# Performance work log

Measured on AMD Instinct MI355X. Metric: run time of the kernel, lower is better.

## Reference

```python
import jax, jax.numpy as jnp
import numpy as np

N, E, D, B, C = 50000, 800000, 128, 20000, 40
EPS_BN = 1e-3    # keras BatchNormalization default epsilon
EPS_NRM = 1e-12  # keras ops.nn.normalize epsilon
FFN_DIMS = {"pre": (D, D), "c1p": (D, D), "c1u": (2 * D, D), "c2p": (D, D), "c2u": (2 * D, D), "post": (D, D)}


def setup_inputs() -> dict:
    key = jax.random.key(0)
    ks = jax.random.split(key, 8)
    inp = {
        "node_features": jax.random.normal(ks[0], (N, D), jnp.float32),
        "edges": jax.random.randint(ks[1], (2, E), 0, N, dtype=jnp.int32),
        "edge_w": jax.random.uniform(ks[2], (E,), jnp.float32),
        "input_node_idx": jax.random.randint(ks[3], (B,), 0, N, dtype=jnp.int32),
    }
    for i, (name, (din, dout)) in enumerate(FFN_DIMS.items()):
        kw = jax.random.fold_in(key, 100 + i)
        inp[name + "_g"] = jnp.ones((din,), jnp.float32)
        inp[name + "_be"] = jnp.zeros((din,), jnp.float32)
        inp[name + "_mu"] = jnp.zeros((din,), jnp.float32)
        inp[name + "_var"] = jnp.ones((din,), jnp.float32)
        inp[name + "_w"] = jax.random.normal(kw, (din, dout), jnp.float32) * (1.0 / float(np.sqrt(din)))
        inp[name + "_bi"] = jnp.zeros((dout,), jnp.float32)
    inp["logits_w"] = jax.random.normal(ks[4], (D, C), jnp.float32) * (1.0 / float(np.sqrt(D)))
    inp["logits_b"] = jnp.zeros((C,), jnp.float32)
    return inp


def ffn(x, g, be, mu, var, w, bi):
    # BatchNorm (inference running stats) -> Dropout (identity) -> Dense + exact gelu
    xn = (x - mu) * jax.lax.rsqrt(var + EPS_BN) * g + be
    return jax.nn.gelu(xn @ w + bi, approximate=False)


def l2norm(x):
    n = jnp.sqrt(jnp.sum(x * x, axis=-1, keepdims=True))
    return x / jnp.maximum(n, EPS_NRM)


def graph_conv(x, node_idx, nbr_idx, ew, prep, upd):
    # gather neighbours -> prepare FFN -> edge-weighted -> segment_sum (reduce='sum')
    msgs = ffn(x[nbr_idx], *prep) * ew[:, None]                         # [E, D]
    red = jax.ops.segment_sum(msgs, node_idx, num_segments=x.shape[0])  # [N, D]
    h = jnp.concatenate([x, red], axis=1)                               # [N, 2D] (combination='concat')
    return l2norm(ffn(h, *upd))                                         # normalize=True


def reference(node_features, edges, edge_w, input_node_idx,
              pre_g, pre_be, pre_mu, pre_var, pre_w, pre_bi,
              c1p_g, c1p_be, c1p_mu, c1p_var, c1p_w, c1p_bi,
              c1u_g, c1u_be, c1u_mu, c1u_var, c1u_w, c1u_bi,
              c2p_g, c2p_be, c2p_mu, c2p_var, c2p_w, c2p_bi,
              c2u_g, c2u_be, c2u_mu, c2u_var, c2u_w, c2u_bi,
              post_g, post_be, post_mu, post_var, post_w, post_bi,
              logits_w, logits_b):
    ew = edge_w / jnp.sum(edge_w)                       # edge_W normalized at init
    node_idx, nbr_idx = edges[0], edges[1]
    x = ffn(node_features, pre_g, pre_be, pre_mu, pre_var, pre_w, pre_bi)
    x = graph_conv(x, node_idx, nbr_idx, ew,
                   (c1p_g, c1p_be, c1p_mu, c1p_var, c1p_w, c1p_bi),
                   (c1u_g, c1u_be, c1u_mu, c1u_var, c1u_w, c1u_bi)) + x
    x = graph_conv(x, node_idx, nbr_idx, ew,
                   (c2p_g, c2p_be, c2p_mu, c2p_var, c2p_w, c2p_bi),
                   (c2u_g, c2u_be, c2u_mu, c2u_var, c2u_w, c2u_bi)) + x
    x = ffn(x, post_g, post_be, post_mu, post_var, post_w, post_bi)
    return x[input_node_idx] @ logits_w + logits_b      # [B, C]
```

## Files before the change

kernel.cpp:

```cpp
#include <hip/hip_runtime.h>
#include <hip/hip_fp16.h>
#include <math.h>

static constexpr int D = 128;
static constexpr int CAP = 64;
static constexpr float EPS_BN = 1e-3f;

typedef short short8 __attribute__((ext_vector_type(8)));
typedef short short4v __attribute__((ext_vector_type(4)));
typedef float float4v __attribute__((ext_vector_type(4)));

__device__ __forceinline__ float gelu_exact(float x) {
    return 0.5f * x * (1.0f + erff(x * 0.70710678118654752f));
}

__device__ __forceinline__ void f32_to_hilo(float f, short& h, short& l) {
    unsigned u = __float_as_uint(f);
    h = (short)(u >> 16);
    float hf = __uint_as_float(u & 0xFFFF0000u);
    unsigned lu = __float_as_uint(f - hf);
    l = (short)(lu >> 16);
}

__device__ __forceinline__ short f32_to_bf16_rne(float f) {
    unsigned u = __float_as_uint(f);
    u += 0x7FFFu + ((u >> 16) & 1u);
    return (short)(u >> 16);
}

__global__ void k_fill_bucket(const int* __restrict__ edges, const float* __restrict__ ew,
                              int* __restrict__ cnt, float* __restrict__ sums,
                              unsigned* __restrict__ cw, int E) {
    int e = blockIdx.x * blockDim.x + threadIdx.x;
    float s = 0.f;
    if (e < E) {
        int dst = edges[e], src = edges[E + e];
        float w = ew[e];
        s = w;
        unsigned short wb = __half_as_ushort(__float2half(w));
        int idx = atomicAdd(&cnt[dst], 1);
        if (idx < CAP)
            cw[(size_t)dst * CAP + idx] = ((unsigned)src << 16) | (unsigned)wb;
    }
    for (int off = 32; off > 0; off >>= 1) s += __shfl_down(s, off, 64);
    __shared__ float sm[4];
    int lane = threadIdx.x & 63, wv = threadIdx.x >> 6;
    if (lane == 0) sm[wv] = s;
    __syncthreads();
    if (threadIdx.x == 0) atomicAdd(sums, sm[0] + sm[1] + sm[2] + sm[3]);
}

struct FoldArgs {
    const float* g[6]; const float* be[6]; const float* mu[6];
    const float* var[6]; const float* w[6]; const float* bi[6];
    short* wh[6]; short* wl[6]; float* bp[6]; int K[6];
};

__global__ void k_fold_all(FoldArgs fa) {
    const int f = blockIdx.y;
    const int c = blockIdx.x;
    const int K = fa.K[f];
    const float* g = fa.g[f]; const float* be = fa.be[f];
    const float* mu = fa.mu[f]; const float* var = fa.var[f];
    const float* w = fa.w[f]; const float* bi = fa.bi[f];
    short* wh = fa.wh[f]; short* wl = fa.wl[f]; float* bp = fa.bp[f];
    float part = 0.f;
    for (int k = threadIdx.x; k < K; k += blockDim.x) {
        float a = g[k] / sqrtf(var[k] + EPS_BN);
        float wv = w[k * D + c];
        float prod = a * wv;
        short hh, ll;
        f32_to_hilo(prod, hh, ll);
        wh[c * K + k] = hh;
        wl[c * K + k] = ll;
        part += (be[k] - mu[k] * a) * wv;
    }
    for (int off = 32; off > 0; off >>= 1) part += __shfl_down(part, off, 64);
    __shared__ float sm[4];
    int lane = threadIdx.x & 63, wv_ = threadIdx.x >> 6;
    if (lane == 0) sm[wv_] = part;
    __syncthreads();
    if (threadIdx.x == 0) bp[c] = bi[c] + sm[0] + sm[1] + sm[2] + sm[3];
}

__global__ void k_reduce(const int* __restrict__ cnt, const unsigned* __restrict__ cw,
                         const float* __restrict__ sums, const __half* __restrict__ y,
                         float* __restrict__ red, int N) {
    int n = blockIdx.x * (blockDim.x >> 6) + (threadIdx.x >> 6);
    if (n >= N) return;
    float inv = 1.0f / sums[0];
    int lane = threadIdx.x & 63;
    int sub = lane >> 4;
    int q = lane & 15;
    int count = min(cnt[n], CAP);
    int start = n * CAP;
    int end = start + count;
    float acc[8] = {0.f, 0.f, 0.f, 0.f, 0.f, 0.f, 0.f, 0.f};
    int i = start + sub;
    if (i < end) {
        unsigned c = cw[i];
        for (;;) {
            int ni = i + 4;
            unsigned nc = 0;
            if (ni < end) nc = cw[ni];
            int src = (int)(c >> 16);
            float w = __half2float(__ushort_as_half((unsigned short)(c & 0xFFFFu))) * inv;
            float4 raw = *((const float4*)(y + (size_t)src * D) + q);
            const __half2* hp = (const __half2*)&raw;
            #pragma unroll
            for (int t = 0; t < 4; t++) {
                float2 f = __half22float2(hp[t]);
                acc[t * 2]     += w * f.x;
                acc[t * 2 + 1] += w * f.y;
            }
            if (ni >= end) break;
            i = ni; c = nc;
        }
    }
    #pragma unroll
    for (int t = 0; t < 8; t++) {
        acc[t] += __shfl_xor(acc[t], 16, 64);
        acc[t] += __shfl_xor(acc[t], 32, 64);
    }
    if (sub == 0) {
        float4 o0 = {acc[0], acc[1], acc[2], acc[3]};
        float4 o1 = {acc[4], acc[5], acc[6], acc[7]};
        *((float4*)(red + (size_t)n * D + q * 8)) = o0;
        *((float4*)(red + (size_t)n * D + q * 8 + 4)) = o1;
    }
}

template<int K, bool L2RES, bool OUT16, bool SPLIT3>
__device__ __forceinline__ void ffn_body(
    short (*__restrict__ Abuf)[128][72], short (*__restrict__ Wbuf)[128][72],
    float (*__restrict__ rs)[2],
    const float* __restrict__ A0, const float* __restrict__ A1,
    const short* __restrict__ Wh, const short* __restrict__ Wl,
    const float* __restrict__ bp, const float* __restrict__ resid,
    float* __restrict__ outf, __half* __restrict__ outh, int nrows)
{
    const int tid = threadIdx.x;
    const int lane = tid & 63;
    const int wv = tid >> 6;
    const int wr = wv >> 1;
    const int wc = wv & 1;
    const int m = lane & 15;
    const int quad = lane >> 4;
    const int rowBlock = blockIdx.x * 128;

    float4v acc[4][4];
    #pragma unroll
    for (int ti = 0; ti < 4; ti++)
        #pragma unroll
        for (int tj = 0; tj < 4; tj++)
            acc[ti][tj] = (float4v){0.f, 0.f, 0.f, 0.f};

    for (int cc = 0; cc < K / 64; cc++) {
        const float* Asrc = (K == 256 && cc >= 2) ? A1 : A0;
        const int kb = (K == 256) ? ((cc & 1) * 64) : (cc * 64);
        const int kw = cc * 64;

        #pragma unroll
        for (int t = 0; t < 8; t++) {
            int i = tid + t * 256;
            int r = i >> 4, k4 = i & 15;
            int grow = rowBlock + r; if (grow >= nrows) grow = nrows - 1;
            float4 f = *((const float4*)(Asrc + (size_t)grow * D + kb) + k4);
            if (SPLIT3) {
                short h0, l0, h1, l1, h2, l2, h3, l3;
                f32_to_hilo(f.x, h0, l0);
                f32_to_hilo(f.y, h1, l1);
                f32_to_hilo(f.z, h2, l2);
                f32_to_hilo(f.w, h3, l3);
                short4v hh = {h0, h1, h2, h3};
                short4v ll = {l0, l1, l2, l3};
                *(short4v*)&Abuf[0][r][k4 * 4] = hh;
                *(short4v*)&Abuf[1][r][k4 * 4] = ll;
            } else {
                short4v hh = {f32_to_bf16_rne(f.x), f32_to_bf16_rne(f.y),
                              f32_to_bf16_rne(f.z), f32_to_bf16_rne(f.w)};
                *(short4v*)&Abuf[0][r][k4 * 4] = hh;
            }
        }
        #pragma unroll
        for (int t = 0; t < 4; t++) {
            int i = tid + t * 256;
            int c = i >> 3, g = i & 7;
            short8 wh8 = *(const short8*)(Wh + (size_t)c * K + kw + g * 8);
            *(short8*)&Wbuf[0][c][g * 8] = wh8;
            if (SPLIT3) {
                short8 wl8 = *(const short8*)(Wl + (size_t)c * K + kw + g * 8);
                *(short8*)&Wbuf[1][c][g * 8] = wl8;
            }
        }
        __syncthreads();

        #pragma unroll
        for (int ks = 0; ks < 2; ks++) {
            short8 ah[4], bh[4];
            #pragma unroll
            for (int ti = 0; ti < 4; ti++)
                ah[ti] = *(const short8*)&Abuf[0][wr * 64 + ti * 16 + m][ks * 32 + quad * 8];
            #pragma unroll
            for (int tj = 0; tj < 4; tj++)
                bh[tj] = *(const short8*)&Wbuf[0][wc * 64 + tj * 16 + m][ks * 32 + quad * 8];
            if (SPLIT3) {
                short8 al[4], bl[4];
                #pragma unroll
                for (int ti = 0; ti < 4; ti++)
                    al[ti] = *(const short8*)&Abuf[1][wr * 64 + ti * 16 + m][ks * 32 + quad * 8];
                #pragma unroll
                for (int tj = 0; tj < 4; tj++)
                    bl[tj] = *(const short8*)&Wbuf[1][wc * 64 + tj * 16 + m][ks * 32 + quad * 8];
                #pragma unroll
                for (int ti = 0; ti < 4; ti++)
                    #pragma unroll
                    for (int tj = 0; tj < 4; tj++) {
                        acc[ti][tj] = __builtin_amdgcn_mfma_f32_16x16x32_bf16(al[ti], bh[tj], acc[ti][tj], 0, 0, 0);
                        acc[ti][tj] = __builtin_amdgcn_mfma_f32_16x16x32_bf16(ah[ti], bl[tj], acc[ti][tj], 0, 0, 0);
                        acc[ti][tj] = __builtin_amdgcn_mfma_f32_16x16x32_bf16(ah[ti], bh[tj], acc[ti][tj], 0, 0, 0);
                    }
            } else {
                #pragma unroll
                for (int ti = 0; ti < 4; ti++)
                    #pragma unroll
                    for (int tj = 0; tj < 4; tj++)
                        acc[ti][tj] = __builtin_amdgcn_mfma_f32_16x16x32_bf16(ah[ti], bh[tj], acc[ti][tj], 0, 0, 0);
            }
        }
        __syncthreads();
    }

    float bvv[4];
    #pragma unroll
    for (int tj = 0; tj < 4; tj++) bvv[tj] = bp[wc * 64 + tj * 16 + m];

    float g[4][4][4];
    #pragma unroll
    for (int ti = 0; ti < 4; ti++)
        #pragma unroll
        for (int tj = 0; tj < 4; tj++)
            #pragma unroll
            for (int r4 = 0; r4 < 4; r4++)
                g[ti][tj][r4] = gelu_exact(acc[ti][tj][r4] + bvv[tj]);

    if (L2RES) {
        #pragma unroll
        for (int ti = 0; ti < 4; ti++)
            #pragma unroll
            for (int r4 = 0; r4 < 4; r4++) {
                float ss = 0.f;
                #pragma unroll
                for (int tj = 0; tj < 4; tj++) ss += g[ti][tj][r4] * g[ti][tj][r4];
                ss += __shfl_xor(ss, 1, 64);
                ss += __shfl_xor(ss, 2, 64);
                ss += __shfl_xor(ss, 4, 64);
                ss += __shfl_xor(ss, 8, 64);
                if (m == 0) rs[wr * 64 + ti * 16 + quad * 4 + r4][wc] = ss;
            }
        __syncthreads();
        #pragma unroll
        for (int ti = 0; ti < 4; ti++)
            #pragma unroll
            for (int r4 = 0; r4 < 4; r4++) {
                int rib = wr * 64 + ti * 16 + quad * 4 + r4;
                float tot = rs[rib][0] + rs[rib][1];
                float inv = 1.0f / fmaxf(sqrtf(tot), 1e-12f);
                int row = rowBlock + rib;
                if (row < nrows) {
                    #pragma unroll
                    for (int tj = 0; tj < 4; tj++) {
                        int c = wc * 64 + tj * 16 + m;
                        outf[(size_t)row * D + c] = g[ti][tj][r4] * inv + resid[(size_t)row * D + c];
                    }
                }
            }
    } else {
        #pragma unroll
        for (int ti = 0; ti < 4; ti++)
            #pragma unroll
            for (int r4 = 0; r4 < 4; r4++) {
                int row = rowBlock + wr * 64 + ti * 16 + quad * 4 + r4;
                if (row < nrows) {
                    #pragma unroll
                    for (int tj = 0; tj < 4; tj++) {
                        int c = wc * 64 + tj * 16 + m;
                        if (OUT16) outh[(size_t)row * D + c] = __float2half(g[ti][tj][r4]);
                        else       outf[(size_t)row * D + c] = g[ti][tj][r4];
                    }
                }
            }
    }
}

__global__ __launch_bounds__(256, 2) void k_pair1(
    const float* __restrict__ nf,
    const short* __restrict__ Wh0, const short* __restrict__ Wl0, const float* __restrict__ Bp0,
    float* __restrict__ xA,
    const short* __restrict__ Wh1, const float* __restrict__ Bp1,
    __half* __restrict__ yh, int N)
{
    __shared__ short Abuf[2][128][72];
    __shared__ short Wbuf[2][128][72];
    __shared__ float rs[128][2];
    ffn_body<128, false, false, true>(Abuf, Wbuf, rs, nf, nullptr, Wh0, Wl0, Bp0, nullptr, xA, nullptr, N);
    __syncthreads();
    ffn_body<128, false, true, false>(Abuf, Wbuf, rs, xA, nullptr, Wh1, nullptr, Bp1, nullptr, nullptr, yh, N);
}

__global__ __launch_bounds__(256, 2) void k_pair2(
    const float* __restrict__ xA, const float* __restrict__ red,
    const short* __restrict__ Wh2, const short* __restrict__ Wl2, const float* __restrict__ Bp2,
    float* __restrict__ y,
    const short* __restrict__ Wh3, const float* __restrict__ Bp3,
    __half* __restrict__ yh, int N)
{
    __shared__ short Abuf[2][128][72];
    __shared__ short Wbuf[2][128][72];
    __shared__ float rs[128][2];
    ffn_body<256, true, false, true>(Abuf, Wbuf, rs, xA, red, Wh2, Wl2, Bp2, xA, y, nullptr, N);
    __syncthreads();
    ffn_body<128, false, true, false>(Abuf, Wbuf, rs, y, nullptr, Wh3, nullptr, Bp3, nullptr, nullptr, yh, N);
}

__global__ __launch_bounds__(256, 2) void k_pair3(
    const float* __restrict__ y, const float* __restrict__ red_in,
    const short* __restrict__ Wh4, const short* __restrict__ Wl4, const float* __restrict__ Bp4,
    float* __restrict__ xA,
    const short* __restrict__ Wh5, const short* __restrict__ Wl5, const float* __restrict__ Bp5,
    float* __restrict__ yout, int N)
{
    __shared__ short Abuf[2][128][72];
    __shared__ short Wbuf[2][128][72];
    __shared__ float rs[128][2];
    ffn_body<256, true, false, true>(Abuf, Wbuf, rs, y, red_in, Wh4, Wl4, Bp4, y, xA, nullptr, N);
    __syncthreads();
    ffn_body<128, false, false, true>(Abuf, Wbuf, rs, xA, nullptr, Wh5, Wl5, Bp5, nullptr, yout, nullptr, N);
}

__global__ void k_logits(const float* __restrict__ x, const int* __restrict__ idx,
                         const float* __restrict__ LW, const float* __restrict__ lb,
                         float* __restrict__ out, int B) {
    int wid = blockIdx.x * 4 + (threadIdx.x >> 6);
    int lane = threadIdx.x & 63;
    if (wid >= B) return;
    int row = __builtin_amdgcn_readfirstlane(idx[wid]);
    if (lane >= 40) return;
    float acc = lb[lane];
    const float4* xr = (const float4*)(x + (size_t)row * D);
    #pragma unroll 4
    for (int k4 = 0; k4 < 32; k4++) {
        float4 xv = xr[k4];
        acc += xv.x * LW[(4 * k4 + 0) * 40 + lane];
        acc += xv.y * LW[(4 * k4 + 1) * 40 + lane];
        acc += xv.z * LW[(4 * k4 + 2) * 40 + lane];
        acc += xv.w * LW[(4 * k4 + 3) * 40 + lane];
    }
    out[(size_t)wid * 40 + lane] = acc;
}

extern "C" void kernel_launch(void* const* d_in, const int* in_sizes, int n_in,
                              void* d_out, int out_size, void* d_ws, size_t ws_size,
                              hipStream_t stream) {
    const float* node_features = (const float*)d_in[0];
    const int*   edges         = (const int*)d_in[1];
    const float* edge_w        = (const float*)d_in[2];
    const int*   input_idx     = (const int*)d_in[3];
    const int N = in_sizes[0] / D;
    const int E = in_sizes[2];
    const int B = in_sizes[3];

    const float* P[6][6];
    for (int f = 0; f < 6; f++)
        for (int q = 0; q < 6; q++)
            P[f][q] = (const float*)d_in[4 + f * 6 + q];
    const float* logits_w = (const float*)d_in[40];
    const float* logits_b = (const float*)d_in[41];

    float* ws = (float*)d_ws;
    size_t nd = (size_t)N * D;
    float* xA  = ws;
    float* y   = ws + nd;
    float* red = ws + 2 * nd;
    float* p   = ws + 3 * nd;
    __half* yh = (__half*)p; p += nd / 2;
    const int Ks[6] = {128, 128, 256, 128, 256, 128};
    short* Wh[6]; short* Wl[6]; float* Bp[6];
    {
        short* sp = (short*)p;
        for (int f = 0; f < 6; f++) {
            Wh[f] = sp; sp += (size_t)Ks[f] * D;
            Wl[f] = sp; sp += (size_t)Ks[f] * D;
        }
        p = (float*)sp;
    }
    for (int f = 0; f < 6; f++) { Bp[f] = p; p += D; }
    int* cnt    = (int*)p; p += N;
    float* sums = p; p += 2;
    unsigned* cw = (unsigned*)p; p += (size_t)N * CAP;

    hipMemsetAsync(cnt, 0, ((size_t)N + 2) * sizeof(int), stream);
    k_fill_bucket<<<(E + 255) / 256, 256, 0, stream>>>(edges, edge_w, cnt, sums, cw, E);

    FoldArgs fa;
    for (int f = 0; f < 6; f++) {
        fa.g[f] = P[f][0]; fa.be[f] = P[f][1]; fa.mu[f] = P[f][2];
        fa.var[f] = P[f][3]; fa.w[f] = P[f][4]; fa.bi[f] = P[f][5];
        fa.wh[f] = Wh[f]; fa.wl[f] = Wl[f]; fa.bp[f] = Bp[f]; fa.K[f] = Ks[f];
    }
    k_fold_all<<<dim3(D, 6), 256, 0, stream>>>(fa);

    const int gb = (N + 127) / 128;
    const int rb = (N + 3) / 4;

    k_pair1<<<gb, 256, 0, stream>>>(node_features, Wh[0], Wl[0], Bp[0], xA, Wh[1], Bp[1], yh, N);
    k_reduce<<<rb, 256, 0, stream>>>(cnt, cw, sums, yh, red, N);
    k_pair2<<<gb, 256, 0, stream>>>(xA, red, Wh[2], Wl[2], Bp[2], y, Wh[3], Bp[3], yh, N);
    k_reduce<<<rb, 256, 0, stream>>>(cnt, cw, sums, yh, red, N);
    k_pair3<<<gb, 256, 0, stream>>>(y, red, Wh[4], Wl[4], Bp[4], xA, Wh[5], Wl[5], Bp[5], red, N);
    k_logits<<<(B + 3) / 4, 256, 0, stream>>>(red, input_idx, logits_w, logits_b, (float*)d_out, B);
}
```

Before: 436.7 us.

## Merge edge bucketing and weight folding into one kernel with destination-partitioned fill

Combines the edge bucket-fill kernel and the BN/weight folding kernel into a single launch, with the first 1024 blocks doing the fill and the remaining 768 doing the folding. The fill is restructured into 8 groups, each scanning every edge but handling only destinations in its own node range. The aim is to keep the atomics and scattered writes of each group within a smaller region of memory and to save one launch. In exchange, the edge and destination arrays are read 8 times.

After: 411.8 us. -5.7%, faster.

```diff
diff --git a/kernel.cpp b/kernel.cpp
--- a/kernel.cpp
+++ b/kernel.cpp
@@ -28,59 +28,71 @@
     return (short)(u >> 16);
 }
 
-__global__ void k_fill_bucket(const int* __restrict__ edges, const float* __restrict__ ew,
-                              int* __restrict__ cnt, float* __restrict__ sums,
-                              unsigned* __restrict__ cw, int E) {
-    int e = blockIdx.x * blockDim.x + threadIdx.x;
-    float s = 0.f;
-    if (e < E) {
-        int dst = edges[e], src = edges[E + e];
-        float w = ew[e];
-        s = w;
-        unsigned short wb = __half_as_ushort(__float2half(w));
-        int idx = atomicAdd(&cnt[dst], 1);
-        if (idx < CAP)
-            cw[(size_t)dst * CAP + idx] = ((unsigned)src << 16) | (unsigned)wb;
-    }
-    for (int off = 32; off > 0; off >>= 1) s += __shfl_down(s, off, 64);
-    __shared__ float sm[4];
-    int lane = threadIdx.x & 63, wv = threadIdx.x >> 6;
-    if (lane == 0) sm[wv] = s;
-    __syncthreads();
-    if (threadIdx.x == 0) atomicAdd(sums, sm[0] + sm[1] + sm[2] + sm[3]);
-}
-
 struct FoldArgs {
     const float* g[6]; const float* be[6]; const float* mu[6];
     const float* var[6]; const float* w[6]; const float* bi[6];
     short* wh[6]; short* wl[6]; float* bp[6]; int K[6];
 };
 
-__global__ void k_fold_all(FoldArgs fa) {
-    const int f = blockIdx.y;
-    const int c = blockIdx.x;
-    const int K = fa.K[f];
-    const float* g = fa.g[f]; const float* be = fa.be[f];
-    const float* mu = fa.mu[f]; const float* var = fa.var[f];
-    const float* w = fa.w[f]; const float* bi = fa.bi[f];
-    short* wh = fa.wh[f]; short* wl = fa.wl[f]; float* bp = fa.bp[f];
-    float part = 0.f;
-    for (int k = threadIdx.x; k < K; k += blockDim.x) {
-        float a = g[k] / sqrtf(var[k] + EPS_BN);
-        float wv = w[k * D + c];
-        float prod = a * wv;
-        short hh, ll;
-        f32_to_hilo(prod, hh, ll);
-        wh[c * K + k] = hh;
-        wl[c * K + k] = ll;
-        part += (be[k] - mu[k] * a) * wv;
-    }
-    for (int off = 32; off > 0; off >>= 1) part += __shfl_down(part, off, 64);
+__global__ void k_build(const int* __restrict__ edges, const float* __restrict__ ew,
+                        int* __restrict__ cnt, float* __restrict__ sums,
+                        unsigned* __restrict__ cw, FoldArgs fa, int E, int N, int fillBlocks) {
     __shared__ float sm[4];
-    int lane = threadIdx.x & 63, wv_ = threadIdx.x >> 6;
-    if (lane == 0) sm[wv_] = part;
-    __syncthreads();
-    if (threadIdx.x == 0) bp[c] = bi[c] + sm[0] + sm[1] + sm[2] + sm[3];
+    const int tid = threadIdx.x;
+    const int lane = tid & 63, wvi = tid >> 6;
+
+    if ((int)blockIdx.x < fillBlocks) {
+        const int g = blockIdx.x & 7;
+        const int bid = blockIdx.x >> 3;
+        const int gstride = (fillBlocks >> 3) * 256;
+        const int N8 = (N + 7) >> 3;
+        const int lo = g * N8;
+        const int hi = min(lo + N8, N);
+        float s = 0.f;
+        for (int e = bid * 256 + tid; e < E; e += gstride) {
+            int dst = edges[e];
+            if (dst >= lo && dst < hi) {
+                int src = edges[E + e];
+                float w = ew[e];
+                s += w;
+                unsigned short wb = __half_as_ushort(__float2half(w));
+                int idx = atomicAdd(&cnt[dst], 1);
+                if (idx < CAP)
+                    cw[(size_t)dst * CAP + idx] = ((unsigned)src << 16) | (unsigned)wb;
+            }
+        }
+        for (int off = 32; off > 0; off >>= 1) s += __shfl_down(s, off, 64);
+        if (lane == 0) sm[wvi] = s;
+        __syncthreads();
+        if (tid == 0) {
+            float t = sm[0] + sm[1] + sm[2] + sm[3];
+            if (t != 0.f) atomicAdd(sums, t);
+        }
+    } else {
+        const int idx = blockIdx.x - fillBlocks;
+        const int f = idx >> 7;
+        const int c = idx & 127;
+        const int K = fa.K[f];
+        const float* g = fa.g[f]; const float* be = fa.be[f];
+        const float* mu = fa.mu[f]; const float* var = fa.var[f];
+        const float* w = fa.w[f]; const float* bi = fa.bi[f];
+        short* wh = fa.wh[f]; short* wl = fa.wl[f]; float* bp = fa.bp[f];
+        float part = 0.f;
+        for (int k = tid; k < K; k += blockDim.x) {
+            float a = g[k] / sqrtf(var[k] + EPS_BN);
+            float wv = w[k * D + c];
+            float prod = a * wv;
+            short hh, ll;
+            f32_to_hilo(prod, hh, ll);
+            wh[c * K + k] = hh;
+            wl[c * K + k] = ll;
+            part += (be[k] - mu[k] * a) * wv;
+        }
+        for (int off = 32; off > 0; off >>= 1) part += __shfl_down(part, off, 64);
+        if (lane == 0) sm[wvi] = part;
+        __syncthreads();
+        if (tid == 0) bp[c] = bi[c] + sm[0] + sm[1] + sm[2] + sm[3];
+    }
 }
 
 __global__ void k_reduce(const int* __restrict__ cnt, const unsigned* __restrict__ cw,
@@ -399,16 +411,16 @@
     float* sums = p; p += 2;
     unsigned* cw = (unsigned*)p; p += (size_t)N * CAP;
 
-    hipMemsetAsync(cnt, 0, ((size_t)N + 2) * sizeof(int), stream);
-    k_fill_bucket<<<(E + 255) / 256, 256, 0, stream>>>(edges, edge_w, cnt, sums, cw, E);
-
     FoldArgs fa;
     for (int f = 0; f < 6; f++) {
         fa.g[f] = P[f][0]; fa.be[f] = P[f][1]; fa.mu[f] = P[f][2];
         fa.var[f] = P[f][3]; fa.w[f] = P[f][4]; fa.bi[f] = P[f][5];
         fa.wh[f] = Wh[f]; fa.wl[f] = Wl[f]; fa.bp[f] = Bp[f]; fa.K[f] = Ks[f];
     }
-    k_fold_all<<<dim3(D, 6), 256, 0, stream>>>(fa);
+
+    const int fillBlocks = 1024;
+    hipMemsetAsync(cnt, 0, ((size_t)N + 2) * sizeof(int), stream);
+    k_build<<<fillBlocks + 768, 256, 0, stream>>>(edges, edge_w, cnt, sums, cw, fa, E, N, fillBlocks);
 
     const int gb = (N + 127) / 128;
     const int rb = (N + 3) / 4;
```
